# Performance work log

Measured on AMD Instinct MI355X. Metric: run time of the kernel, lower is better.

## Reference

```python
import jax, jax.numpy as jnp
import numpy as np

WEIGHT = 1.0  # init kwarg `weight`
BOX = 5      # half-size of the text box in pixels


def setup_inputs() -> dict:
    key = jax.random.key(0)
    k1, k2, k3, k4 = jax.random.split(key, 4)
    B, C, H, W, T = 32, 4, 512, 512, 64
    return {
        "predicted_noise": jax.random.normal(k1, (B, C, H, W), dtype=jnp.float32),
        "target_noise": jax.random.normal(k2, (B, C, H, W), dtype=jnp.float32),
        "text_tokens": jax.random.randint(k3, (B, T), 0, 50000, dtype=jnp.int64),
        "text_positions": jax.random.uniform(k4, (B, T, 2), dtype=jnp.float32),
    }


def _text_mask(text_positions, H, W, dtype):
    # text_positions: [B, T, 2] normalized (x, y). A valid token (x>0, y>0)
    # paints a [y_pos-5, y_pos+5) x [x_pos-5, x_pos+5) box of ones (clipped to image).
    x = text_positions[..., 0]
    y = text_positions[..., 1]
    valid = (x > 0) & (y > 0)                              # [B, T]
    x_pos = jnp.floor(x * W).astype(jnp.int32)             # int(x*W), x>0 so floor==trunc
    y_pos = jnp.floor(y * H).astype(jnp.int32)
    ii = jnp.arange(H, dtype=jnp.int32)                    # rows; clipping is implicit
    jj = jnp.arange(W, dtype=jnp.int32)
    cond_y = valid[..., None] & (ii >= y_pos[..., None] - BOX) & (ii < y_pos[..., None] + BOX)  # [B,T,H]
    cond_x = (jj >= x_pos[..., None] - BOX) & (jj < x_pos[..., None] + BOX)                      # [B,T,W]
    # union over tokens of the outer-product boxes, via a small matmul over T
    hits = jnp.einsum('bti,btj->bij', cond_y.astype(dtype), cond_x.astype(dtype))  # [B,H,W]
    return (hits > 0).astype(dtype)


def reference(predicted_noise, target_noise, text_tokens, text_positions):
    diff2 = (predicted_noise - target_noise) ** 2
    base_loss = jnp.mean(diff2)
    _, _, H, W = predicted_noise.shape
    mask = _text_mask(text_positions, H, W, predicted_noise.dtype)   # [B,H,W]
    text_weight = 1.0 + 3.0 * mask[:, None, :, :]                    # [B,1,H,W]
    text_loss = jnp.mean(text_weight * diff2)
    return base_loss + WEIGHT * (text_loss - base_loss)
```

## Files before the change

kernel.cpp:

```cpp
#include <hip/hip_runtime.h>

#define Bb 32
#define Cc 4
#define Hh 512
#define Ww 512
#define Tt 64
#define HW (Hh * Ww)
#define NTOT ((long long)Bb * Cc * Hh * Ww)
#define NQUAD (Bb * HW / 4)
#define NBLOCKS (NQUAD / 256)

#define ROWMASK_OFF 65536

__global__ __launch_bounds__(256) void build_rowmask_kernel(
    const float* __restrict__ pos,
    unsigned long long* __restrict__ rowmask)
{
    int row = blockIdx.x * 256 + threadIdx.x;
    if (row >= Bb * Hh) return;
    int b = row >> 9;
    int h = row & 511;

    unsigned long long m[8];
#pragma unroll
    for (int i = 0; i < 8; ++i) m[i] = 0ull;

    const float* p = pos + (size_t)b * Tt * 2;
    for (int t = 0; t < Tt; ++t) {
        float x = p[2 * t + 0];
        float y = p[2 * t + 1];
        if (!(x > 0.0f && y > 0.0f)) continue;
        int xp = (int)floorf(x * (float)Ww);
        int yp = (int)floorf(y * (float)Hh);
        if (h < yp - 5 || h >= yp + 5) continue;
        int xlo = xp - 5; if (xlo < 0) xlo = 0;
        int xhi = xp + 5; if (xhi > Ww) xhi = Ww;
        if (xlo >= xhi) continue;
        int w0 = xlo >> 6;
        int w1 = (xhi - 1) >> 6;
        for (int wd = w0; wd <= w1; ++wd) {
            int lo = xlo - (wd << 6); if (lo < 0) lo = 0;
            int hi = xhi - (wd << 6); if (hi > 64) hi = 64;
            m[wd] |= (((1ull << (hi - lo)) - 1ull) << lo);
        }
    }

    unsigned long long* out = rowmask + (size_t)row * 8;
#pragma unroll
    for (int i = 0; i < 8; ++i) out[i] = m[i];
}

__global__ __launch_bounds__(256) void weighted_sq_sum_kernel(
    const float* __restrict__ pred,
    const float* __restrict__ targ,
    const unsigned long long* __restrict__ rowmask,
    double* __restrict__ partials)
{
    int gid = blockIdx.x * 256 + threadIdx.x;
    int b   = gid >> 16;
    int rem = gid & 65535;
    int h   = rem >> 7;
    int wq  = rem & 127;
    int w   = wq << 2;

    size_t base = (size_t)b * (Cc * HW) + (size_t)h * Ww + (size_t)w;
    const float4* p4 = (const float4*)(pred + base);
    const float4* t4 = (const float4*)(targ + base);
    const int PS = HW / 4;

    unsigned long long word = rowmask[((size_t)b * Hh + h) * 8 + (w >> 6)];
    int shift = w & 63;

    float sx = 0.f, sy = 0.f, sz = 0.f, sw = 0.f;
#pragma unroll
    for (int c = 0; c < Cc; ++c) {
        float4 a = p4[(size_t)c * PS];
        float4 t = t4[(size_t)c * PS];
        float dx = a.x - t.x, dy = a.y - t.y, dz = a.z - t.z, dw = a.w - t.w;
        sx += dx * dx; sy += dy * dy; sz += dz * dz; sw += dw * dw;
    }

    float tot  = sx + sy + sz + sw;
    float msum = 0.f;
    msum += ((word >> (shift + 0)) & 1ull) ? sx : 0.f;
    msum += ((word >> (shift + 1)) & 1ull) ? sy : 0.f;
    msum += ((word >> (shift + 2)) & 1ull) ? sz : 0.f;
    msum += ((word >> (shift + 3)) & 1ull) ? sw : 0.f;

    double v = (double)tot + 3.0 * (double)msum;

#pragma unroll
    for (int off = 32; off > 0; off >>= 1)
        v += __shfl_down(v, off, 64);

    __shared__ double lsum[4];
    int lane = threadIdx.x & 63;
    int wid  = threadIdx.x >> 6;
    if (lane == 0) lsum[wid] = v;
    __syncthreads();
    if (threadIdx.x == 0)
        partials[blockIdx.x] = lsum[0] + lsum[1] + lsum[2] + lsum[3];
}

__global__ __launch_bounds__(256) void final_reduce_kernel(
    const double* __restrict__ partials, float* __restrict__ out)
{
    double v = 0.0;
    for (int i = threadIdx.x; i < NBLOCKS; i += 256) v += partials[i];
#pragma unroll
    for (int off = 32; off > 0; off >>= 1)
        v += __shfl_down(v, off, 64);
    __shared__ double lsum[4];
    int lane = threadIdx.x & 63;
    int wid  = threadIdx.x >> 6;
    if (lane == 0) lsum[wid] = v;
    __syncthreads();
    if (threadIdx.x == 0)
        out[0] = (float)((lsum[0] + lsum[1] + lsum[2] + lsum[3]) * (1.0 / (double)NTOT));
}

extern "C" void kernel_launch(void* const* d_in, const int* in_sizes, int n_in,
                              void* d_out, int out_size, void* d_ws, size_t ws_size,
                              hipStream_t stream) {
    const float* pred = (const float*)d_in[0];
    const float* targ = (const float*)d_in[1];
    const float* pos  = (const float*)d_in[3];

    double* partials = (double*)d_ws;
    unsigned long long* rowmask =
        (unsigned long long*)((char*)d_ws + ROWMASK_OFF);
    float* out = (float*)d_out;

    build_rowmask_kernel<<<(Bb * Hh + 255) / 256, 256, 0, stream>>>(pos, rowmask);

    weighted_sq_sum_kernel<<<NBLOCKS, 256, 0, stream>>>(pred, targ, rowmask, partials);

    final_reduce_kernel<<<1, 256, 0, stream>>>(partials, out);
}
```

Baseline: 293.7 us.

## Fuse final reduction via last-block atomic counter and batch quads per thread

Each thread in the main reduction kernel now handles four quads in a grid-stride pattern over 2048 blocks instead of one quad per thread over many more blocks. The separate final reduce launch is removed: the last block to finish, detected with an atomic counter, sums the partials. The row-mask build now stages token boxes in shared memory with one block per batch. The aim is to cut launch overhead and the per-block reduction cost, and to get more bytes in flight per thread, at the cost of atomic release/acquire ordering and a counter reset inside the mask kernel.

```diff
diff --git a/kernel.cpp b/kernel.cpp
--- a/kernel.cpp
+++ b/kernel.cpp
@@ -8,115 +8,157 @@
 #define HW (Hh * Ww)
 #define NTOT ((long long)Bb * Cc * Hh * Ww)
 #define NQUAD (Bb * HW / 4)
-#define NBLOCKS (NQUAD / 256)
+#define GRID 2048
+#define BLOCK 256
+#define QPT 4
+#define STRIDE (GRID * BLOCK)
 
+#define COUNTER_OFF 16384
 #define ROWMASK_OFF 65536
 
 __global__ __launch_bounds__(256) void build_rowmask_kernel(
     const float* __restrict__ pos,
-    unsigned long long* __restrict__ rowmask)
+    unsigned long long* __restrict__ rowmask,
+    unsigned int* __restrict__ counter)
 {
-    int row = blockIdx.x * 256 + threadIdx.x;
-    if (row >= Bb * Hh) return;
-    int b = row >> 9;
-    int h = row & 511;
+    int b   = blockIdx.x;
+    int tid = threadIdx.x;
 
-    unsigned long long m[8];
-#pragma unroll
-    for (int i = 0; i < 8; ++i) m[i] = 0ull;
+    if (b == 0 && tid == 0) *counter = 0u;
 
-    const float* p = pos + (size_t)b * Tt * 2;
-    for (int t = 0; t < Tt; ++t) {
-        float x = p[2 * t + 0];
-        float y = p[2 * t + 1];
-        if (!(x > 0.0f && y > 0.0f)) continue;
-        int xp = (int)floorf(x * (float)Ww);
-        int yp = (int)floorf(y * (float)Hh);
-        if (h < yp - 5 || h >= yp + 5) continue;
+    __shared__ int s_ylo[Tt], s_yhi[Tt], s_xlo[Tt], s_xhi[Tt];
+    if (tid < Tt) {
+        const float2 xy = ((const float2*)pos)[b * Tt + tid];
+        bool valid = (xy.x > 0.0f) && (xy.y > 0.0f);
+        int xp = (int)floorf(xy.x * (float)Ww);
+        int yp = (int)floorf(xy.y * (float)Hh);
         int xlo = xp - 5; if (xlo < 0) xlo = 0;
         int xhi = xp + 5; if (xhi > Ww) xhi = Ww;
-        if (xlo >= xhi) continue;
-        int w0 = xlo >> 6;
-        int w1 = (xhi - 1) >> 6;
-        for (int wd = w0; wd <= w1; ++wd) {
-            int lo = xlo - (wd << 6); if (lo < 0) lo = 0;
-            int hi = xhi - (wd << 6); if (hi > 64) hi = 64;
-            m[wd] |= (((1ull << (hi - lo)) - 1ull) << lo);
+        if (!valid) { xlo = 0; xhi = 0; }
+        s_ylo[tid] = valid ? yp - 5 : (1 << 30);
+        s_yhi[tid] = valid ? yp + 5 : -(1 << 30);
+        s_xlo[tid] = xlo;
+        s_xhi[tid] = xhi;
+    }
+    __syncthreads();
+
+#pragma unroll
+    for (int r = 0; r < 2; ++r) {
+        int h = 2 * tid + r;
+        unsigned long long m[8];
+#pragma unroll
+        for (int i = 0; i < 8; ++i) m[i] = 0ull;
+
+        for (int t = 0; t < Tt; ++t) {
+            if (h < s_ylo[t] || h >= s_yhi[t]) continue;
+            int xlo = s_xlo[t], xhi = s_xhi[t];
+            if (xlo >= xhi) continue;
+            int w0 = xlo >> 6;
+            int w1 = (xhi - 1) >> 6;
+            for (int wd = w0; wd <= w1; ++wd) {
+                int lo = xlo - (wd << 6); if (lo < 0) lo = 0;
+                int hi = xhi - (wd << 6); if (hi > 64) hi = 64;
+                m[wd] |= (((1ull << (hi - lo)) - 1ull) << lo);
+            }
         }
+
+        ulonglong2* out = (ulonglong2*)(rowmask + ((size_t)b * Hh + h) * 8);
+#pragma unroll
+        for (int i = 0; i < 4; ++i)
+            out[i] = make_ulonglong2(m[2 * i], m[2 * i + 1]);
     }
-
-    unsigned long long* out = rowmask + (size_t)row * 8;
-#pragma unroll
-    for (int i = 0; i < 8; ++i) out[i] = m[i];
 }
 
 __global__ __launch_bounds__(256) void weighted_sq_sum_kernel(
     const float* __restrict__ pred,
     const float* __restrict__ targ,
     const unsigned long long* __restrict__ rowmask,
-    double* __restrict__ partials)
+    double* __restrict__ partials,
+    unsigned int* __restrict__ counter,
+    float* __restrict__ out)
 {
-    int gid = blockIdx.x * 256 + threadIdx.x;
-    int b   = gid >> 16;
-    int rem = gid & 65535;
-    int h   = rem >> 7;
-    int wq  = rem & 127;
-    int w   = wq << 2;
+    const int tid  = threadIdx.x;
+    const int base = blockIdx.x * BLOCK + tid;
+    const int PS   = HW / 4;
 
-    size_t base = (size_t)b * (Cc * HW) + (size_t)h * Ww + (size_t)w;
-    const float4* p4 = (const float4*)(pred + base);
-    const float4* t4 = (const float4*)(targ + base);
-    const int PS = HW / 4;
+    double v = 0.0;
 
-    unsigned long long word = rowmask[((size_t)b * Hh + h) * 8 + (w >> 6)];
-    int shift = w & 63;
+#pragma unroll
+    for (int k = 0; k < QPT; ++k) {
+        int q   = base + k * STRIDE;
+        int b   = q >> 16;
+        int rem = q & 65535;
+        int h   = rem >> 7;
+        int wq  = rem & 127;
+        int w   = wq << 2;
 
-    float sx = 0.f, sy = 0.f, sz = 0.f, sw = 0.f;
-#pragma unroll
-    for (int c = 0; c < Cc; ++c) {
-        float4 a = p4[(size_t)c * PS];
-        float4 t = t4[(size_t)c * PS];
-        float dx = a.x - t.x, dy = a.y - t.y, dz = a.z - t.z, dw = a.w - t.w;
+        size_t off = (size_t)b * (Cc * HW) + (size_t)h * Ww + (size_t)w;
+        const float4* p4 = (const float4*)(pred + off);
+        const float4* t4 = (const float4*)(targ + off);
+
+        float4 a0 = p4[0 * PS], a1 = p4[1 * PS], a2 = p4[2 * PS], a3 = p4[3 * PS];
+        float4 b0 = t4[0 * PS], b1 = t4[1 * PS], b2 = t4[2 * PS], b3 = t4[3 * PS];
+        unsigned long long word = rowmask[((size_t)b * Hh + h) * 8 + (w >> 6)];
+        int shift = w & 63;
+
+        float dx, dy, dz, dw;
+        float sx, sy, sz, sw;
+        dx = a0.x - b0.x; dy = a0.y - b0.y; dz = a0.z - b0.z; dw = a0.w - b0.w;
+        sx = dx * dx; sy = dy * dy; sz = dz * dz; sw = dw * dw;
+        dx = a1.x - b1.x; dy = a1.y - b1.y; dz = a1.z - b1.z; dw = a1.w - b1.w;
         sx += dx * dx; sy += dy * dy; sz += dz * dz; sw += dw * dw;
+        dx = a2.x - b2.x; dy = a2.y - b2.y; dz = a2.z - b2.z; dw = a2.w - b2.w;
+        sx += dx * dx; sy += dy * dy; sz += dz * dz; sw += dw * dw;
+        dx = a3.x - b3.x; dy = a3.y - b3.y; dz = a3.z - b3.z; dw = a3.w - b3.w;
+        sx += dx * dx; sy += dy * dy; sz += dz * dz; sw += dw * dw;
+
+        float tot  = sx + sy + sz + sw;
+        float msum = 0.f;
+        msum += ((word >> (shift + 0)) & 1ull) ? sx : 0.f;
+        msum += ((word >> (shift + 1)) & 1ull) ? sy : 0.f;
+        msum += ((word >> (shift + 2)) & 1ull) ? sz : 0.f;
+        msum += ((word >> (shift + 3)) & 1ull) ? sw : 0.f;
+
+        v += (double)tot + 3.0 * (double)msum;
     }
-
-    float tot  = sx + sy + sz + sw;
-    float msum = 0.f;
-    msum += ((word >> (shift + 0)) & 1ull) ? sx : 0.f;
-    msum += ((word >> (shift + 1)) & 1ull) ? sy : 0.f;
-    msum += ((word >> (shift + 2)) & 1ull) ? sz : 0.f;
-    msum += ((word >> (shift + 3)) & 1ull) ? sw : 0.f;
-
-    double v = (double)tot + 3.0 * (double)msum;
 
 #pragma unroll
     for (int off = 32; off > 0; off >>= 1)
         v += __shfl_down(v, off, 64);
 
     __shared__ double lsum[4];
-    int lane = threadIdx.x & 63;
-    int wid  = threadIdx.x >> 6;
+    __shared__ int lastFlag;
+    int lane = tid & 63;
+    int wid  = tid >> 6;
     if (lane == 0) lsum[wid] = v;
     __syncthreads();
-    if (threadIdx.x == 0)
-        partials[blockIdx.x] = lsum[0] + lsum[1] + lsum[2] + lsum[3];
-}
 
-__global__ __launch_bounds__(256) void final_reduce_kernel(
-    const double* __restrict__ partials, float* __restrict__ out)
-{
-    double v = 0.0;
-    for (int i = threadIdx.x; i < NBLOCKS; i += 256) v += partials[i];
+    if (tid == 0) {
+        double p = lsum[0] + lsum[1] + lsum[2] + lsum[3];
+        __hip_atomic_store(&partials[blockIdx.x], p, __ATOMIC_RELEASE,
+                           __HIP_MEMORY_SCOPE_AGENT);
+        unsigned int old = __hip_atomic_fetch_add(counter, 1u, __ATOMIC_ACQ_REL,
+                                                  __HIP_MEMORY_SCOPE_AGENT);
+        lastFlag = (old == (unsigned int)(gridDim.x - 1));
+    }
+    __syncthreads();
+
+    if (lastFlag) {
+        double s = 0.0;
 #pragma unroll
-    for (int off = 32; off > 0; off >>= 1)
-        v += __shfl_down(v, off, 64);
-    __shared__ double lsum[4];
-    int lane = threadIdx.x & 63;
-    int wid  = threadIdx.x >> 6;
-    if (lane == 0) lsum[wid] = v;
-    __syncthreads();
-    if (threadIdx.x == 0)
-        out[0] = (float)((lsum[0] + lsum[1] + lsum[2] + lsum[3]) * (1.0 / (double)NTOT));
+        for (int i = 0; i < GRID / BLOCK; ++i)
+            s += __hip_atomic_load(&partials[i * BLOCK + tid], __ATOMIC_RELAXED,
+                                   __HIP_MEMORY_SCOPE_AGENT);
+#pragma unroll
+        for (int off = 32; off > 0; off >>= 1)
+            s += __shfl_down(s, off, 64);
+        __syncthreads();
+        if (lane == 0) lsum[wid] = s;
+        __syncthreads();
+        if (tid == 0)
+            out[0] = (float)((lsum[0] + lsum[1] + lsum[2] + lsum[3]) *
+                             (1.0 / (double)NTOT));
+    }
 }
 
 extern "C" void kernel_launch(void* const* d_in, const int* in_sizes, int n_in,
@@ -127,13 +169,12 @@
     const float* pos  = (const float*)d_in[3];
 
     double* partials = (double*)d_ws;
+    unsigned int* counter = (unsigned int*)((char*)d_ws + COUNTER_OFF);
     unsigned long long* rowmask =
         (unsigned long long*)((char*)d_ws + ROWMASK_OFF);
     float* out = (float*)d_out;
 
-    build_rowmask_kernel<<<(Bb * Hh + 255) / 256, 256, 0, stream>>>(pos, rowmask);
-
-    weighted_sq_sum_kernel<<<NBLOCKS, 256, 0, stream>>>(pred, targ, rowmask, partials);
-
-    final_reduce_kernel<<<1, 256, 0, stream>>>(partials, out);
+    build_rowmask_kernel<<<Bb, BLOCK, 0, stream>>>(pos, rowmask, counter);
+    weighted_sq_sum_kernel<<<GRID, BLOCK, 0, stream>>>(pred, targ, rowmask,
+                                                       partials, counter, out);
 }
```

Result: slower. 480.7 us (+63.7%).
